# Kernel tuning notes

Hardware: AMD Instinct MI355X
Metric: run time of the kernel (lower is better)

Reference implementation:

```python
import jax, jax.numpy as jnp
import numpy as np

N, E, R, B, IN, H, OUT, P = 20000, 320000, 8, 8, 128, 256, 128, 100000
LN_EPS = 1e-5


def _xavier(key, shape):
    fan_in, fan_out = shape[-2], shape[-1]
    lim = float(np.sqrt(6.0 / (fan_in + fan_out)))
    return jax.random.uniform(key, shape, jnp.float32, -lim, lim)


def setup_inputs() -> dict:
    key = jax.random.key(0)
    ks = iter(jax.random.split(key, 64))
    inp = {}
    inp['x'] = jax.random.normal(next(ks), (N, IN), jnp.float32)
    inp['edge_index'] = jax.random.randint(next(ks), (2, E), 0, N, jnp.int32)
    inp['edge_type'] = jax.random.randint(next(ks), (E,), 0, R, jnp.int32)
    inp['gene_pairs'] = jax.random.randint(next(ks), (2, P), 0, N, jnp.int32)
    dims = [(IN, H), (H, H), (H, H), (H, OUT)]  # per-layer (in_ch, out_ch)
    for i, (ic, oc) in enumerate(dims):
        inp[f'basis{i}'] = _xavier(next(ks), (B, ic, oc))
        inp[f'att{i}'] = _xavier(next(ks), (R, B))
        inp[f'root{i}'] = _xavier(next(ks), (ic, oc))
        inp[f'relatt{i}'] = jnp.ones((R,), jnp.float32)
        inp[f'g{i}'] = jnp.ones((oc,), jnp.float32)
        inp[f'b{i}'] = jnp.zeros((oc,), jnp.float32)
    inp['res0'] = _xavier(next(ks), (IN, H))   # in_ch != out_ch at layer 0
    inp['res3'] = _xavier(next(ks), (H, OUT))  # and at layer 3
    # decoder: 3*OUT -> H -> H//2 -> H//4 -> 1
    ddims = [(3 * OUT, H), (H, H // 2), (H // 2, H // 4), (H // 4, 1)]
    for i, (ic, oc) in enumerate(ddims):
        inp[f'dW{i}'] = _xavier(next(ks), (ic, oc))
        inp[f'db{i}'] = jnp.zeros((oc,), jnp.float32)
        if i < 3:
            inp[f'dg{i}'] = jnp.ones((oc,), jnp.float32)
            inp[f'dbb{i}'] = jnp.zeros((oc,), jnp.float32)
    return inp


def _ln(h, g, b):
    m = h.mean(-1, keepdims=True)
    v = ((h - m) ** 2).mean(-1, keepdims=True)
    return (h - m) * jax.lax.rsqrt(v + LN_EPS) * g + b


def _conv(x, src, dst, et, basis, att, root_w, rel_att):
    # W_r = sum_b att[r,b] * B_b ; message = a_{r(e)} * x_src @ W_{r(e)}
    # Since the message is linear, aggregate x_src per (dst, relation) first
    # (segment_sum), then apply the R small GEMMs once - same math, no [E,in,out].
    n, d = x.shape
    weight = jnp.einsum('rb,bio->rio', att, basis)          # [R,in,out]
    a = jax.nn.softmax(rel_att)                              # [R]
    seg = dst.astype(jnp.int32) * R + et.astype(jnp.int32)   # [(node,rel)] segment ids
    agg = jax.ops.segment_sum(x[src], seg, num_segments=n * R).reshape(n, R, d)
    out = jnp.einsum('nri,rio->no', agg, weight * a[:, None, None])
    return out + x @ root_w


def reference(x, edge_index, edge_type, gene_pairs,
              basis0, att0, root0, relatt0, g0, b0, res0,
              basis1, att1, root1, relatt1, g1, b1,
              basis2, att2, root2, relatt2, g2, b2,
              basis3, att3, root3, relatt3, g3, b3, res3,
              dW0, db0, dg0, dbb0, dW1, db1, dg1, dbb1,
              dW2, db2, dg2, dbb2, dW3, db3):
    src, dst = edge_index[0], edge_index[1]
    layers = [
        (basis0, att0, root0, relatt0, g0, b0, res0),
        (basis1, att1, root1, relatt1, g1, b1, None),
        (basis2, att2, root2, relatt2, g2, b2, None),
        (basis3, att3, root3, relatt3, g3, b3, res3),
    ]
    h = x
    for i, (bs, at, rt, ra, g, b, res) in enumerate(layers):
        h_in = h
        h = _conv(h, src, dst, edge_type, bs, at, rt, ra)
        h = _ln(h, g, b)
        h = h + (h_in @ res if res is not None else h_in)
        if i < len(layers) - 1:
            h = jax.nn.gelu(h, approximate=False)
    z = h  # [N, OUT]
    zi, zj = z[gene_pairs[0]], z[gene_pairs[1]]
    pe = jnp.concatenate([zi + zj, zi * zj, jnp.abs(zi - zj)], axis=-1)
    d = jax.nn.gelu(_ln(pe @ dW0 + db0, dg0, dbb0), approximate=False)
    d = jax.nn.gelu(_ln(d @ dW1 + db1, dg1, dbb1), approximate=False)
    d = jax.nn.gelu(_ln(d @ dW2 + db2, dg2, dbb2), approximate=False)
    logits = (d @ dW3 + db3).squeeze(-1)  # [P]
    return logits, z
```

## Files before the change

kernel.cpp:

```cpp
#include <hip/hip_runtime.h>
#include <hip/hip_bf16.h>
#include <math.h>
#include <cstddef>
#include <stdint.h>

#define NN 20000
#define EE 320000
#define RR 8
#define PP 100000
#define NR (NN * RR)

typedef __hip_bfloat16 bf16;
typedef __attribute__((ext_vector_type(8))) short short8;
typedef __attribute__((ext_vector_type(4))) short short4v;
typedef __attribute__((ext_vector_type(4))) float floatx4;

__device__ __forceinline__ float b2f(bf16 v) { return __bfloat162float(v); }
__device__ __forceinline__ bf16 f2b(float v) { return __float2bfloat16(v); }
__device__ __forceinline__ float bits2f(unsigned short u) {
  unsigned int i = ((unsigned int)u) << 16; float f; __builtin_memcpy(&f, &i, 4); return f;
}
__device__ __forceinline__ short f2bits(float f) {
  bf16 h = __float2bfloat16(f); short s; __builtin_memcpy(&s, &h, 2); return s;
}
__device__ __forceinline__ float gelu_f(float y) {
  return 0.5f * y * (1.f + erff(y * 0.7071067811865476f));
}
__device__ __forceinline__ void async_copy16(void* lds, const void* g) {
  __builtin_amdgcn_global_load_lds((const __attribute__((address_space(1))) void*)g,
                                   (__attribute__((address_space(3))) void*)lds, 16, 0, 0);
}
__device__ __forceinline__ const short8* frag_at(const bf16* base, int row, int q) {
  return (const short8*)(base + row * 64 + (((q) ^ (row & 7)) << 3));
}
__device__ __forceinline__ const short8* frag256(const bf16* base, int row, int col64, int q) {
  return (const short8*)(base + row * 256 + col64 + (((q) ^ (row & 7)) << 3));
}
__device__ __forceinline__ int idx128(int row, int qg) {
  return row * 128 + ((qg >> 3) << 6) + (((qg & 7) ^ (row & 7)) << 3);
}

__global__ void hist_k(const int* __restrict__ dst, const int* __restrict__ et,
                       int* __restrict__ counts) {
  int e = blockIdx.x * 256 + threadIdx.x;
  if (e >= EE) return;
  atomicAdd(&counts[dst[e] * RR + et[e]], 1);
}

__global__ void scan1_k(const int* __restrict__ counts, int* __restrict__ prefix,
                        int* __restrict__ bsums) {
  __shared__ int tmp[256];
  int i = blockIdx.x * 256 + threadIdx.x;
  int v = counts[i];
  tmp[threadIdx.x] = v; __syncthreads();
  for (int off = 1; off < 256; off <<= 1) {
    int x = (threadIdx.x >= off) ? tmp[threadIdx.x - off] : 0;
    __syncthreads();
    tmp[threadIdx.x] += x;
    __syncthreads();
  }
  prefix[i] = tmp[threadIdx.x] - v;
  if (threadIdx.x == 255) bsums[blockIdx.x] = tmp[255];
}

__global__ void scan2_k(int* __restrict__ bsums, int nb) {
  __shared__ int tmp[256];
  __shared__ int carry;
  if (threadIdx.x == 0) carry = 0;
  __syncthreads();
  for (int base = 0; base < nb; base += 256) {
    int i = base + threadIdx.x;
    int v = (i < nb) ? bsums[i] : 0;
    tmp[threadIdx.x] = v; __syncthreads();
    for (int off = 1; off < 256; off <<= 1) {
      int x = (threadIdx.x >= off) ? tmp[threadIdx.x - off] : 0;
      __syncthreads();
      tmp[threadIdx.x] += x;
      __syncthreads();
    }
    int c = carry;
    if (i < nb) bsums[i] = c + tmp[threadIdx.x] - v;
    __syncthreads();
    if (threadIdx.x == 255) carry = c + tmp[255];
    __syncthreads();
  }
}

__global__ void scan3_k(int* __restrict__ prefix, const int* __restrict__ bsums) {
  int i = blockIdx.x * 256 + threadIdx.x;
  prefix[i] += bsums[blockIdx.x];
}

__global__ void scatter_k(const int* __restrict__ src, const int* __restrict__ dst,
                          const int* __restrict__ et, const int* __restrict__ segstart,
                          int* __restrict__ cursor, int* __restrict__ ssrc) {
  int e = blockIdx.x * 256 + threadIdx.x;
  if (e >= EE) return;
  int s = dst[e] * RR + et[e];
  int pos = atomicAdd(&cursor[s], 1);
  ssrc[segstart[s] + pos] = src[e];
}

__global__ void cvt_bf16_k(const float* __restrict__ in, bf16* __restrict__ out, int n) {
  int i = blockIdx.x * 256 + threadIdx.x;
  if (i < n) out[i] = f2b(in[i]);
}

__global__ void softmax4_k(const float* r0, const float* r1, const float* r2,
                           const float* r3, float* __restrict__ a) {
  if (threadIdx.x == 0) {
    const float* rs[4] = {r0, r1, r2, r3};
    for (int l = 0; l < 4; ++l) {
      float mx = -1e30f;
      for (int i = 0; i < RR; ++i) mx = fmaxf(mx, rs[l][i]);
      float e[RR]; float s = 0.f;
      for (int i = 0; i < RR; ++i) { e[i] = expf(rs[l][i] - mx); s += e[i]; }
      for (int i = 0; i < RR; ++i) a[l * RR + i] = e[i] / s;
    }
  }
}

__global__ void transpose_k(const float* __restrict__ in, bf16* __restrict__ out,
                            int rows, int cols) {
  int idx = blockIdx.x * 256 + threadIdx.x;
  if (idx >= rows * cols) return;
  int r = idx / cols, c = idx - r * cols;
  out[(size_t)c * rows + r] = f2b(in[idx]);
}

__global__ void prep_w_k(const float* __restrict__ basis, const float* __restrict__ att,
                         const float* __restrict__ root, const float* __restrict__ a,
                         bf16* __restrict__ Wt, int ic, int icsh, int oc, int ocsh) {
  int idx = blockIdx.x * 256 + threadIdx.x;
  int cols = 9 * ic;
  if (idx >= cols * oc) return;
  int o = idx & (oc - 1);
  int col = idx >> ocsh;
  int r = col >> icsh;
  int k = col & (ic - 1);
  float val;
  if (r < RR) {
    float acc = 0.f;
    for (int bb = 0; bb < RR; ++bb)
      acc += att[r * RR + bb] * basis[((size_t)bb * ic + k) * oc + o];
    val = a[r] * acc;
  } else {
    val = root[(size_t)k * oc + o];
  }
  Wt[(size_t)o * cols + col] = f2b(val);
}

__global__ __launch_bounds__(256) void aggregate_k(
    const bf16* __restrict__ h, const int* __restrict__ segstart,
    const int* __restrict__ counts, const int* __restrict__ ssrc,
    bf16* __restrict__ agg, int ic, int tpnsh) {
  int tpn = 1 << tpnsh;
  int npb = 256 >> tpnsh;
  int local = threadIdx.x >> tpnsh;
  int n = blockIdx.x * npb + local;
  if (n >= NN) return;
  int cbase = (threadIdx.x & (tpn - 1)) * 8;
  size_t rowoff = (size_t)n * (9 * ic);
  for (int r = 0; r < RR; ++r) {
    int s = n * RR + r;
    int st = segstart[s];
    int cnt = counts[s];
    float a[8] = {0.f, 0.f, 0.f, 0.f, 0.f, 0.f, 0.f, 0.f};
    for (int i = 0; i < cnt; ++i) {
      int src = ssrc[st + i];
      short8 v = *(const short8*)(h + (size_t)src * ic + cbase);
#pragma unroll
      for (int j = 0; j < 8; ++j) a[j] += bits2f((unsigned short)v[j]);
    }
    short8 o;
#pragma unroll
    for (int j = 0; j < 8; ++j) o[j] = f2bits(a[j]);
    *(short8*)(agg + rowoff + r * ic + cbase) = o;
  }
  *(short8*)(agg + rowoff + 8 * ic + cbase) =
      *(const short8*)(h + (size_t)n * ic + cbase);
}

__global__ __launch_bounds__(256) void gemm_f32_k(
    const bf16* __restrict__ A, const bf16* __restrict__ Wt,
    float* __restrict__ Cf, int M, int N, int K, int nb) {
  const int bid = blockIdx.x;
  const int xcd = bid & 7;
  const int slot = bid >> 3;
  const int gidx = slot / nb;
  const int member = slot - gidx * nb;
  const int mb = (M + 127) >> 7;
  const int m = gidx * 8 + xcd;
  if (m >= mb) return;
  const int m0 = m * 128;
  const int n0 = member * 64;

  __shared__ __align__(16) bf16 As[128 * 64];
  __shared__ __align__(16) bf16 Ws[64 * 64];
  const int tid = threadIdx.x;
  const int wave = tid >> 6, lane = tid & 63;
  const int quad = lane >> 4, l16 = lane & 15;
  const int wm = (wave >> 1) * 64, wn = (wave & 1) * 32;
  floatx4 acc[4][2];
#pragma unroll
  for (int i = 0; i < 4; ++i)
#pragma unroll
    for (int j = 0; j < 2; ++j) acc[i][j] = (floatx4){0.f, 0.f, 0.f, 0.f};

  for (int k0 = 0; k0 < K; k0 += 64) {
#pragma unroll
    for (int q = 0; q < 4; ++q) {
      int c0 = (wave * 4 + q) * 1024;
      int row = (c0 >> 7) + (lane >> 3);
      int grow = m0 + row; if (grow >= M) grow = M - 1;
      int ch = (lane & 7) ^ (row & 7);
      async_copy16((char*)As + c0, A + (size_t)grow * K + k0 + ch * 8);
    }
#pragma unroll
    for (int q = 0; q < 2; ++q) {
      int c0 = (wave * 2 + q) * 1024;
      int row = (c0 >> 7) + (lane >> 3);
      int ch = (lane & 7) ^ (row & 7);
      async_copy16((char*)Ws + c0, Wt + (size_t)(n0 + row) * K + k0 + ch * 8);
    }
    __syncthreads();
#pragma unroll
    for (int kk = 0; kk < 64; kk += 32) {
      int qb = (kk >> 3) + quad;
      short8 b0 = *frag_at(Ws, wn + l16, qb);
      short8 b1 = *frag_at(Ws, wn + 16 + l16, qb);
#pragma unroll
      for (int i = 0; i < 4; ++i) {
        short8 a = *frag_at(As, wm + i * 16 + l16, qb);
        acc[i][0] = __builtin_amdgcn_mfma_f32_16x16x32_bf16(a, b0, acc[i][0], 0, 0, 0);
        acc[i][1] = __builtin_amdgcn_mfma_f32_16x16x32_bf16(a, b1, acc[i][1], 0, 0, 0);
      }
    }
    __syncthreads();
  }
#pragma unroll
  for (int i = 0; i < 4; ++i)
#pragma unroll
    for (int j = 0; j < 2; ++j)
#pragma unroll
      for (int r = 0; r < 4; ++r) {
        int row = m0 + wm + i * 16 + quad * 4 + r;
        int col = n0 + wn + j * 16 + l16;
        if (row < M) Cf[(size_t)row * N + col] = acc[i][j][r];
      }
}

__global__ __launch_bounds__(256) void gemm_plain_k(
    const bf16* __restrict__ A, const bf16* __restrict__ Wt,
    bf16* __restrict__ Cb, int M, int N, int K) {
  __shared__ __align__(16) bf16 As[64 * 64];
  __shared__ __align__(16) bf16 Ws[64 * 64];
  const int m0 = blockIdx.y * 64;
  const int n0 = blockIdx.x * 64;
  const int tid = threadIdx.x;
  const int wave = tid >> 6, lane = tid & 63;
  const int quad = lane >> 4, l16 = lane & 15;
  const int wm = (wave >> 1) * 32, wn = (wave & 1) * 32;
  floatx4 acc00 = {0.f, 0.f, 0.f, 0.f};
  floatx4 acc01 = acc00, acc10 = acc00, acc11 = acc00;

  for (int k0 = 0; k0 < K; k0 += 64) {
#pragma unroll
    for (int q = 0; q < 2; ++q) {
      int c0 = (wave * 2 + q) * 1024;
      int row = (c0 >> 7) + (lane >> 3);
      int grow = m0 + row; if (grow >= M) grow = M - 1;
      int ch = (lane & 7) ^ (row & 7);
      async_copy16((char*)As + c0, A + (size_t)grow * K + k0 + ch * 8);
    }
#pragma unroll
    for (int q = 0; q < 2; ++q) {
      int c0 = (wave * 2 + q) * 1024;
      int row = (c0 >> 7) + (lane >> 3);
      int ch = (lane & 7) ^ (row & 7);
      async_copy16((char*)Ws + c0, Wt + (size_t)(n0 + row) * K + k0 + ch * 8);
    }
    __syncthreads();
#pragma unroll
    for (int kk = 0; kk < 64; kk += 32) {
      int qb = (kk >> 3) + quad;
      short8 a0 = *frag_at(As, wm + l16, qb);
      short8 a1 = *frag_at(As, wm + 16 + l16, qb);
      short8 b0 = *frag_at(Ws, wn + l16, qb);
      short8 b1 = *frag_at(Ws, wn + 16 + l16, qb);
      acc00 = __builtin_amdgcn_mfma_f32_16x16x32_bf16(a0, b0, acc00, 0, 0, 0);
      acc01 = __builtin_amdgcn_mfma_f32_16x16x32_bf16(a0, b1, acc01, 0, 0, 0);
      acc10 = __builtin_amdgcn_mfma_f32_16x16x32_bf16(a1, b0, acc10, 0, 0, 0);
      acc11 = __builtin_amdgcn_mfma_f32_16x16x32_bf16(a1, b1, acc11, 0, 0, 0);
    }
    __syncthreads();
  }
  floatx4 accs[2][2] = {{acc00, acc01}, {acc10, acc11}};
#pragma unroll
  for (int i = 0; i < 2; ++i)
#pragma unroll
    for (int j = 0; j < 2; ++j)
#pragma unroll
      for (int r = 0; r < 4; ++r) {
        int row = m0 + wm + i * 16 + quad * 4 + r;
        int col = n0 + wn + j * 16 + l16;
        if (row < M) Cb[(size_t)row * N + col] = f2b(accs[i][j][r]);
      }
}

__global__ __launch_bounds__(256) void ln_conv_k(
    const float* __restrict__ conv, const bf16* __restrict__ res,
    const float* __restrict__ g, const float* __restrict__ b,
    bf16* __restrict__ out, float* __restrict__ zout, int oc, int do_gelu) {
  int wave = threadIdx.x >> 6, lane = threadIdx.x & 63;
  int row = blockIdx.x * 4 + wave;
  if (row >= NN) return;
  int ne = oc >> 6;
  float v[4];
  float s = 0.f, s2 = 0.f;
  for (int i = 0; i < ne; ++i) {
    v[i] = conv[(size_t)row * oc + i * 64 + lane];
    s += v[i]; s2 += v[i] * v[i];
  }
  for (int off = 32; off; off >>= 1) { s += __shfl_xor(s, off); s2 += __shfl_xor(s2, off); }
  float m = s / oc;
  float var = s2 / oc - m * m;
  float rs = rsqrtf(var + 1e-5f);
  for (int i = 0; i < ne; ++i) {
    int c = i * 64 + lane;
    float y = (v[i] - m) * rs * g[c] + b[c];
    y += b2f(res[(size_t)row * oc + c]);
    if (zout) zout[(size_t)row * oc + c] = y;
    if (do_gelu) y = gelu_f(y);
    out[(size_t)row * oc + c] = f2b(y);
  }
}

__global__ __launch_bounds__(256) void gemm_pe_k(
    const bf16* __restrict__ z, const int* __restrict__ pairs,
    const bf16* __restrict__ WAT, const bf16* __restrict__ WBT,
    const bf16* __restrict__ WCT,
    bf16* __restrict__ P0) {
  __shared__ __align__(16) bf16 PEs[128 * 64];
  __shared__ __align__(16) bf16 Ws[64 * 64];
  const int tid = threadIdx.x;
  const int wave = tid >> 6, lane = tid & 63;
  const int quad = lane >> 4, l16 = lane & 15;
  const int wm = (wave >> 1) * 64, wn = (wave & 1) * 32;
  const int m0 = blockIdx.y * 128;
  const int n0 = blockIdx.x * 64;

  const int prow = tid >> 1;
  const int colq = (tid & 1) * 32;
  int pp = m0 + prow; if (pp >= PP) pp = PP - 1;
  const bf16* zi = z + (size_t)pairs[pp] * 128;
  const bf16* zj = z + (size_t)pairs[PP + pp] * 128;

  floatx4 acc[4][2];
#pragma unroll
  for (int i = 0; i < 4; ++i)
#pragma unroll
    for (int j = 0; j < 2; ++j) acc[i][j] = (floatx4){0.f, 0.f, 0.f, 0.f};

#pragma unroll
  for (int kwi = 0; kwi < 2; ++kwi) {
    const int kw = kwi * 64;
    short8 va[4], vb[4];
#pragma unroll
    for (int c8 = 0; c8 < 4; ++c8) {
      va[c8] = *(const short8*)(zi + kw + colq + c8 * 8);
      vb[c8] = *(const short8*)(zj + kw + colq + c8 * 8);
    }
#pragma unroll
    for (int op = 0; op < 3; ++op) {
      const bf16* W = (op == 0) ? WAT : (op == 1) ? WBT : WCT;
#pragma unroll
      for (int q = 0; q < 2; ++q) {
        int c0 = q * 4096 + wave * 1024;
        int row = (c0 >> 7) + (lane >> 3);
        int ch = (lane & 7) ^ (row & 7);
        async_copy16((char*)Ws + c0, W + (size_t)(n0 + row) * 128 + kw + ch * 8);
      }
#pragma unroll
      for (int c8 = 0; c8 < 4; ++c8) {
        short8 o;
#pragma unroll
        for (int jj = 0; jj < 8; ++jj) {
          float fa = bits2f((unsigned short)va[c8][jj]);
          float fb = bits2f((unsigned short)vb[c8][jj]);
          float v = (op == 0) ? (fa + fb) : (op == 1) ? (fa * fb) : fabsf(fa - fb);
          o[jj] = f2bits(v);
        }
        int q = (tid & 1) * 4 + c8;
        *(short8*)(PEs + prow * 64 + ((q ^ (prow & 7)) << 3)) = o;
      }
      __syncthreads();
#pragma unroll
      for (int kk = 0; kk < 64; kk += 32) {
        int qb = (kk >> 3) + quad;
        short8 b0 = *frag_at(Ws, wn + l16, qb);
        short8 b1 = *frag_at(Ws, wn + 16 + l16, qb);
#pragma unroll
        for (int i = 0; i < 4; ++i) {
          short8 a = *frag_at(PEs, wm + i * 16 + l16, qb);
          acc[i][0] = __builtin_amdgcn_mfma_f32_16x16x32_bf16(a, b0, acc[i][0], 0, 0, 0);
          acc[i][1] = __builtin_amdgcn_mfma_f32_16x16x32_bf16(a, b1, acc[i][1], 0, 0, 0);
        }
      }
      __syncthreads();
    }
  }

#pragma unroll
  for (int i = 0; i < 4; ++i)
#pragma unroll
    for (int j = 0; j < 2; ++j)
#pragma unroll
      for (int r = 0; r < 4; ++r) {
        int row = m0 + wm + i * 16 + quad * 4 + r;
        int col = n0 + wn + j * 16 + l16;
        if (row < PP) P0[(size_t)row * 256 + col] = f2b(acc[i][j][r]);
      }
}

__global__ __launch_bounds__(256) void ln_d0_k(bf16* __restrict__ D0,
                                               const float* __restrict__ db0,
                                               const float* __restrict__ g,
                                               const float* __restrict__ b) {
  int wave = threadIdx.x >> 6, lane = threadIdx.x & 63;
  int row = blockIdx.x * 4 + wave;
  if (row >= PP) return;
  bf16* p = D0 + (size_t)row * 256 + lane * 4;
  short4v xv = *(const short4v*)p;
  float v[4];
  float s = 0.f, s2 = 0.f;
#pragma unroll
  for (int k = 0; k < 4; ++k) {
    v[k] = bits2f((unsigned short)xv[k]) + db0[lane * 4 + k];
    s += v[k]; s2 += v[k] * v[k];
  }
  for (int off = 32; off; off >>= 1) { s += __shfl_xor(s, off); s2 += __shfl_xor(s2, off); }
  float m = s / 256.f;
  float var = s2 / 256.f - m * m;
  float rs = rsqrtf(var + 1e-5f);
  short4v ov;
#pragma unroll
  for (int k = 0; k < 4; ++k) {
    int c = lane * 4 + k;
    float y = (v[k] - m) * rs * g[c] + b[c];
    ov[k] = f2bits(gelu_f(y));
  }
  *(short4v*)p = ov;
}

__global__ __launch_bounds__(256) void lngemm1_k(
    const bf16* __restrict__ D0, const bf16* __restrict__ W1t,
    const float* __restrict__ bias, bf16* __restrict__ P1, int M) {
  __shared__ __align__(16) bf16 As[64 * 256];
  __shared__ __align__(16) bf16 Ws[128 * 64];
  const int tid = threadIdx.x;
  const int wave = tid >> 6, lane = tid & 63;
  const int quad = lane >> 4, l16 = lane & 15;
  const int wr = (wave >> 1) * 32;
  const int wc = (wave & 1) * 64;
  const int m0 = blockIdx.x * 64;

  {
    const int srow = tid >> 2;
    const int q4 = tid & 3;
    int grow = m0 + srow; if (grow >= M) grow = M - 1;
    const bf16* src = D0 + (size_t)grow * 256 + q4 * 64;
#pragma unroll
    for (int c8 = 0; c8 < 8; ++c8) {
      short8 o = *(const short8*)(src + c8 * 8);
      *(short8*)(As + srow * 256 + q4 * 64 + ((c8 ^ (srow & 7)) << 3)) = o;
    }
  }

  floatx4 acc[2][4];
#pragma unroll
  for (int i = 0; i < 2; ++i)
#pragma unroll
    for (int j = 0; j < 4; ++j) acc[i][j] = (floatx4){0.f, 0.f, 0.f, 0.f};

  for (int kc = 0; kc < 4; ++kc) {
#pragma unroll
    for (int q = 0; q < 4; ++q) {
      int c0 = q * 4096 + wave * 1024;
      int row = (c0 >> 7) + (lane >> 3);
      int ch = (lane & 7) ^ (row & 7);
      async_copy16((char*)Ws + c0, W1t + (size_t)row * 256 + kc * 64 + ch * 8);
    }
    __syncthreads();
#pragma unroll
    for (int kk = 0; kk < 64; kk += 32) {
      int qb = (kk >> 3) + quad;
      short8 a0 = *frag256(As, wr + l16, kc * 64, qb);
      short8 a1 = *frag256(As, wr + 16 + l16, kc * 64, qb);
#pragma unroll
      for (int j = 0; j < 4; ++j) {
        short8 bb = *frag_at(Ws, wc + j * 16 + l16, qb);
        acc[0][j] = __builtin_amdgcn_mfma_f32_16x16x32_bf16(a0, bb, acc[0][j], 0, 0, 0);
        acc[1][j] = __builtin_amdgcn_mfma_f32_16x16x32_bf16(a1, bb, acc[1][j], 0, 0, 0);
      }
    }
    __syncthreads();
  }

#pragma unroll
  for (int i = 0; i < 2; ++i)
#pragma unroll
    for (int r = 0; r < 4; ++r) {
      int row = wr + i * 16 + quad * 4 + r;
      int grow = m0 + row;
      if (grow >= M) continue;
#pragma unroll
      for (int j = 0; j < 4; ++j) {
        int col = wc + j * 16 + l16;
        P1[(size_t)grow * 128 + col] = f2b(acc[i][j][r] + bias[col]);
      }
    }
}

__global__ __launch_bounds__(256) void lngemm2_k(
    const bf16* __restrict__ P1, const bf16* __restrict__ W2t,
    const float* __restrict__ g, const float* __restrict__ b,
    const float* __restrict__ bias, bf16* __restrict__ P2, int M) {
  __shared__ __align__(16) bf16 As[64 * 128];
  __shared__ __align__(16) bf16 Ws[64 * 64];
  const int tid = threadIdx.x;
  const int wave = tid >> 6, lane = tid & 63;
  const int quad = lane >> 4, l16 = lane & 15;
  const int m0 = blockIdx.x * 64;

  {
    const int srow = tid >> 2;
    const int q4 = tid & 3;
    int grow = m0 + srow; if (grow >= M) grow = M - 1;
    const bf16* src = P1 + (size_t)grow * 128 + q4 * 32;
    float v[32];
    float s = 0.f, s2 = 0.f;
#pragma unroll
    for (int c8 = 0; c8 < 4; ++c8) {
      short8 x = *(const short8*)(src + c8 * 8);
#pragma unroll
      for (int jj = 0; jj < 8; ++jj) {
        float f = bits2f((unsigned short)x[jj]);
        v[c8 * 8 + jj] = f; s += f; s2 += f * f;
      }
    }
    s += __shfl_xor(s, 1); s2 += __shfl_xor(s2, 1);
    s += __shfl_xor(s, 2); s2 += __shfl_xor(s2, 2);
    float mean = s / 128.f;
    float var = s2 / 128.f - mean * mean;
    float rs = rsqrtf(var + 1e-5f);
#pragma unroll
    for (int c8 = 0; c8 < 4; ++c8) {
      short8 o;
#pragma unroll
      for (int jj = 0; jj < 8; ++jj) {
        int col = q4 * 32 + c8 * 8 + jj;
        float y = (v[c8 * 8 + jj] - mean) * rs * g[col] + b[col];
        o[jj] = f2bits(gelu_f(y));
      }
      *(short8*)(As + idx128(srow, q4 * 4 + c8)) = o;
    }
  }

  floatx4 acc[4];
#pragma unroll
  for (int j = 0; j < 4; ++j) acc[j] = (floatx4){0.f, 0.f, 0.f, 0.f};

  for (int kc = 0; kc < 2; ++kc) {
#pragma unroll
    for (int q = 0; q < 2; ++q) {
      int c0 = q * 4096 + wave * 1024;
      int row = (c0 >> 7) + (lane >> 3);
      int ch = (lane & 7) ^ (row & 7);
      async_copy16((char*)Ws + c0, W2t + (size_t)row * 128 + kc * 64 + ch * 8);
    }
    __syncthreads();
#pragma unroll
    for (int kk = 0; kk < 64; kk += 32) {
      int qb = (kk >> 3) + quad;
      short8 a = *(const short8*)(As + idx128(wave * 16 + l16, kc * 8 + qb));
#pragma unroll
      for (int j = 0; j < 4; ++j) {
        short8 bb = *frag_at(Ws, j * 16 + l16, qb);
        acc[j] = __builtin_amdgcn_mfma_f32_16x16x32_bf16(a, bb, acc[j], 0, 0, 0);
      }
    }
    __syncthreads();
  }

#pragma unroll
  for (int r = 0; r < 4; ++r) {
    int row = wave * 16 + quad * 4 + r;
    int grow = m0 + row;
    if (grow >= M) continue;
#pragma unroll
    for (int j = 0; j < 4; ++j) {
      int col = j * 16 + l16;
      P2[(size_t)grow * 64 + col] = f2b(acc[j][r] + bias[col]);
    }
  }
}

__global__ __launch_bounds__(256) void logits_k(const bf16* __restrict__ P2,
                                                const float* __restrict__ g,
                                                const float* __restrict__ b,
                                                const float* __restrict__ w3,
                                                const float* __restrict__ b3,
                                                float* __restrict__ out) {
  int wave = threadIdx.x >> 6, lane = threadIdx.x & 63;
  int p = blockIdx.x * 4 + wave;
  if (p >= PP) return;
  float v = b2f(P2[(size_t)p * 64 + lane]);
  float s = v, s2 = v * v;
  for (int off = 32; off; off >>= 1) { s += __shfl_xor(s, off); s2 += __shfl_xor(s2, off); }
  float m = s / 64.f;
  float var = s2 / 64.f - m * m;
  float rs = rsqrtf(var + 1e-5f);
  float y = gelu_f((v - m) * rs * g[lane] + b[lane]);
  float t = y * w3[lane];
  for (int off = 32; off; off >>= 1) t += __shfl_xor(t, off);
  if (lane == 0) out[p] = t + b3[0];
}

extern "C" void kernel_launch(void* const* d_in, const int* in_sizes, int n_in,
                              void* d_out, int out_size, void* d_ws, size_t ws_size,
                              hipStream_t stream) {
  auto cdiv = [](int a, int b) { return (a + b - 1) / b; };

  const float* x = (const float*)d_in[0];
  const int* ei = (const int*)d_in[1];
  const int* et = (const int*)d_in[2];
  const int* gp = (const int*)d_in[3];
  const float *basis[4], *att[4], *root[4], *relatt[4], *gln[4], *bln[4];
  for (int l = 0; l < 4; ++l) {
    basis[l]  = (const float*)d_in[4 + 6 * l];
    att[l]    = (const float*)d_in[5 + 6 * l];
    root[l]   = (const float*)d_in[6 + 6 * l];
    relatt[l] = (const float*)d_in[7 + 6 * l];
    gln[l]    = (const float*)d_in[8 + 6 * l];
    bln[l]    = (const float*)d_in[9 + 6 * l];
  }
  const float* res0 = (const float*)d_in[28];
  const float* res3 = (const float*)d_in[29];
  const float* dW0 = (const float*)d_in[30]; const float* db0 = (const float*)d_in[31];
  const float* dg0 = (const float*)d_in[32]; const float* dbb0 = (const float*)d_in[33];
  const float* dW1 = (const float*)d_in[34]; const float* db1 = (const float*)d_in[35];
  const float* dg1 = (const float*)d_in[36]; const float* dbb1 = (const float*)d_in[37];
  const float* dW2 = (const float*)d_in[38]; const float* db2 = (const float*)d_in[39];
  const float* dg2 = (const float*)d_in[40]; const float* dbb2 = (const float*)d_in[41];
  const float* dW3 = (const float*)d_in[42]; const float* db3 = (const float*)d_in[43];

  char* base = (char*)d_ws;
  size_t off = 0;
  auto alloc = [&](size_t bytes) -> char* {
    char* p = base + off;
    off += (bytes + 255) & ~(size_t)255;
    return p;
  };
  bf16* X16 = (bf16*)alloc((size_t)NN * 128 * 2);
  bf16* HA  = (bf16*)alloc((size_t)NN * 256 * 2);
  bf16* HB  = (bf16*)alloc((size_t)NN * 256 * 2);
  bf16* RESB = (bf16*)alloc((size_t)NN * 256 * 2);
  float* CONV = (float*)alloc((size_t)NN * 256 * 4);
  bf16* WT    = (bf16*)alloc((size_t)589824 * 2);
  bf16* RES0T = (bf16*)alloc((size_t)32768 * 2);
  bf16* RES3T = (bf16*)alloc((size_t)32768 * 2);
  bf16* WAT   = (bf16*)alloc((size_t)32768 * 2);
  bf16* WBT   = (bf16*)alloc((size_t)32768 * 2);
  bf16* WCT   = (bf16*)alloc((size_t)32768 * 2);
  bf16* DW1T  = (bf16*)alloc((size_t)32768 * 2);
  bf16* DW2T  = (bf16*)alloc((size_t)8192 * 2);
  float* ASOFT = (float*)alloc(32 * 4);
  int* COUNTS = (int*)alloc((size_t)NR * 4);
  int* SEG    = (int*)alloc((size_t)NR * 4);
  int* CUR    = (int*)alloc((size_t)NR * 4);
  int* BS     = (int*)alloc(1024 * 4);
  int* SSRC   = (int*)alloc((size_t)EE * 4);
  char* BIG = alloc(93000000);
  bf16* AGG = (bf16*)BIG;
  bf16* D0  = (bf16*)BIG;
  bf16* P1  = (bf16*)alloc((size_t)PP * 128 * 2);
  bf16* P2  = (bf16*)alloc((size_t)PP * 64 * 2);
  (void)ws_size; (void)in_sizes; (void)n_in; (void)out_size;

  float* out_logits = (float*)d_out;
  float* out_z = (float*)d_out + PP;

  hipMemsetAsync(COUNTS, 0, (size_t)NR * 4, stream);
  hipMemsetAsync(CUR, 0, (size_t)NR * 4, stream);
  hist_k<<<cdiv(EE, 256), 256, 0, stream>>>(ei + EE, et, COUNTS);
  scan1_k<<<NR / 256, 256, 0, stream>>>(COUNTS, SEG, BS);
  scan2_k<<<1, 256, 0, stream>>>(BS, NR / 256);
  scan3_k<<<NR / 256, 256, 0, stream>>>(SEG, BS);
  scatter_k<<<cdiv(EE, 256), 256, 0, stream>>>(ei, ei + EE, et, SEG, CUR, SSRC);

  cvt_bf16_k<<<cdiv(NN * 128, 256), 256, 0, stream>>>(x, X16, NN * 128);
  softmax4_k<<<1, 64, 0, stream>>>(relatt[0], relatt[1], relatt[2], relatt[3], ASOFT);
  transpose_k<<<cdiv(128 * 256, 256), 256, 0, stream>>>(res0, RES0T, 128, 256);
  transpose_k<<<cdiv(256 * 128, 256), 256, 0, stream>>>(res3, RES3T, 256, 128);
  transpose_k<<<cdiv(128 * 256, 256), 256, 0, stream>>>(dW0, WAT, 128, 256);
  transpose_k<<<cdiv(128 * 256, 256), 256, 0, stream>>>(dW0 + 128 * 256, WBT, 128, 256);
  transpose_k<<<cdiv(128 * 256, 256), 256, 0, stream>>>(dW0 + 256 * 256, WCT, 128, 256);
  transpose_k<<<cdiv(256 * 128, 256), 256, 0, stream>>>(dW1, DW1T, 256, 128);
  transpose_k<<<cdiv(128 * 64, 256), 256, 0, stream>>>(dW2, DW2T, 128, 64);

  const int mb = cdiv(NN, 128);
  const int swzP4 = 8 * cdiv(mb, 8) * 4;
  const int swzP2 = 8 * cdiv(mb, 8) * 2;

  prep_w_k<<<cdiv(9 * 128 * 256, 256), 256, 0, stream>>>(basis[0], att[0], root[0], ASOFT + 0, WT, 128, 7, 256, 8);
  aggregate_k<<<cdiv(NN, 16), 256, 0, stream>>>(X16, SEG, COUNTS, SSRC, AGG, 128, 4);
  gemm_plain_k<<<dim3(4, cdiv(NN, 64)), 256, 0, stream>>>(X16, RES0T, RESB, NN, 256, 128);
  gemm_f32_k<<<swzP4, 256, 0, stream>>>(AGG, WT, CONV, NN, 256, 1152, 4);
  ln_conv_k<<<cdiv(NN, 4), 256, 0, stream>>>(CONV, RESB, gln[0], bln[0], HA, nullptr, 256, 1);

  prep_w_k<<<cdiv(9 * 256 * 256, 256), 256, 0, stream>>>(basis[1], att[1], root[1], ASOFT + 8, WT, 256, 8, 256, 8);
  aggregate_k<<<cdiv(NN, 8), 256, 0, stream>>>(HA, SEG, COUNTS, SSRC, AGG, 256, 5);
  gemm_f32_k<<<swzP4, 256, 0, stream>>>(AGG, WT, CONV, NN, 256, 2304, 4);
  ln_conv_k<<<cdiv(NN, 4), 256, 0, stream>>>(CONV, HA, gln[1], bln[1], HB, nullptr, 256, 1);

  prep_w_k<<<cdiv(9 * 256 * 256, 256), 256, 0, stream>>>(basis[2], att[2], root[2], ASOFT + 16, WT, 256, 8, 256, 8);
  aggregate_k<<<cdiv(NN, 8), 256, 0, stream>>>(HB, SEG, COUNTS, SSRC, AGG, 256, 5);
  gemm_f32_k<<<swzP4, 256, 0, stream>>>(AGG, WT, CONV, NN, 256, 2304, 4);
  ln_conv_k<<<cdiv(NN, 4), 256, 0, stream>>>(CONV, HB, gln[2], bln[2], HA, nullptr, 256, 1);

  prep_w_k<<<cdiv(9 * 256 * 128, 256), 256, 0, stream>>>(basis[3], att[3], root[3], ASOFT + 24, WT, 256, 8, 128, 7);
  aggregate_k<<<cdiv(NN, 8), 256, 0, stream>>>(HA, SEG, COUNTS, SSRC, AGG, 256, 5);
  gemm_plain_k<<<dim3(2, cdiv(NN, 64)), 256, 0, stream>>>(HA, RES3T, RESB, NN, 128, 256);
  gemm_f32_k<<<swzP2, 256, 0, stream>>>(AGG, WT, CONV, NN, 128, 2304, 2);
  ln_conv_k<<<cdiv(NN, 4), 256, 0, stream>>>(CONV, RESB, gln[3], bln[3], HB, out_z, 128, 0);

  gemm_pe_k<<<dim3(4, cdiv(PP, 128)), 256, 0, stream>>>(HB, gp, WAT, WBT, WCT, D0);
  ln_d0_k<<<cdiv(PP, 4), 256, 0, stream>>>(D0, db0, dg0, dbb0);
  lngemm1_k<<<cdiv(PP, 64), 256, 0, stream>>>(D0, DW1T, db1, P1, PP);
  lngemm2_k<<<cdiv(PP, 64), 256, 0, stream>>>(P1, DW2T, dg1, dbb1, db2, P2, PP);
  logits_k<<<cdiv(PP, 4), 256, 0, stream>>>(P2, dg2, dbb2, dW3, db3, out_logits);
}
```

Baseline: 792.4 us.

## Precompute z@WA per node and remap pair-GEMM grid for XCD locality

```diff
diff --git a/kernel.cpp b/kernel.cpp
--- a/kernel.cpp
+++ b/kernel.cpp
@@ -338,17 +338,25 @@
 
 __global__ __launch_bounds__(256) void gemm_pe_k(
     const bf16* __restrict__ z, const int* __restrict__ pairs,
-    const bf16* __restrict__ WAT, const bf16* __restrict__ WBT,
-    const bf16* __restrict__ WCT,
+    const bf16* __restrict__ WBT, const bf16* __restrict__ WCT,
     bf16* __restrict__ P0) {
+  const int bid = blockIdx.x;
+  const int xcd = bid & 7;
+  const int slot = bid >> 3;
+  const int gidx = slot >> 2;
+  const int member = slot & 3;
+  const int mb = (PP + 127) >> 7;
+  const int m = gidx * 8 + xcd;
+  if (m >= mb) return;
+  const int m0 = m * 128;
+  const int n0 = member * 64;
+
   __shared__ __align__(16) bf16 PEs[128 * 64];
   __shared__ __align__(16) bf16 Ws[64 * 64];
   const int tid = threadIdx.x;
   const int wave = tid >> 6, lane = tid & 63;
   const int quad = lane >> 4, l16 = lane & 15;
   const int wm = (wave >> 1) * 64, wn = (wave & 1) * 32;
-  const int m0 = blockIdx.y * 128;
-  const int n0 = blockIdx.x * 64;
 
   const int prow = tid >> 1;
   const int colq = (tid & 1) * 32;
@@ -372,8 +380,8 @@
       vb[c8] = *(const short8*)(zj + kw + colq + c8 * 8);
     }
 #pragma unroll
-    for (int op = 0; op < 3; ++op) {
-      const bf16* W = (op == 0) ? WAT : (op == 1) ? WBT : WCT;
+    for (int op = 0; op < 2; ++op) {
+      const bf16* W = (op == 0) ? WBT : WCT;
 #pragma unroll
       for (int q = 0; q < 2; ++q) {
         int c0 = q * 4096 + wave * 1024;
@@ -388,7 +396,7 @@
         for (int jj = 0; jj < 8; ++jj) {
           float fa = bits2f((unsigned short)va[c8][jj]);
           float fb = bits2f((unsigned short)vb[c8][jj]);
-          float v = (op == 0) ? (fa + fb) : (op == 1) ? (fa * fb) : fabsf(fa - fb);
+          float v = (op == 0) ? (fa * fb) : fabsf(fa - fb);
           o[jj] = f2bits(v);
         }
         int q = (tid & 1) * 4 + c8;
@@ -424,19 +432,25 @@
 }
 
 __global__ __launch_bounds__(256) void ln_d0_k(bf16* __restrict__ D0,
+                                               const int* __restrict__ pairs,
+                                               const bf16* __restrict__ ZA,
                                                const float* __restrict__ db0,
                                                const float* __restrict__ g,
                                                const float* __restrict__ b) {
   int wave = threadIdx.x >> 6, lane = threadIdx.x & 63;
   int row = blockIdx.x * 4 + wave;
   if (row >= PP) return;
+  int gi = pairs[row], gj = pairs[PP + row];
   bf16* p = D0 + (size_t)row * 256 + lane * 4;
   short4v xv = *(const short4v*)p;
+  short4v av = *(const short4v*)(ZA + (size_t)gi * 256 + lane * 4);
+  short4v bv = *(const short4v*)(ZA + (size_t)gj * 256 + lane * 4);
   float v[4];
   float s = 0.f, s2 = 0.f;
 #pragma unroll
   for (int k = 0; k < 4; ++k) {
-    v[k] = bits2f((unsigned short)xv[k]) + db0[lane * 4 + k];
+    v[k] = bits2f((unsigned short)xv[k]) + bits2f((unsigned short)av[k]) +
+           bits2f((unsigned short)bv[k]) + db0[lane * 4 + k];
     s += v[k]; s2 += v[k] * v[k];
   }
   for (int off = 32; off; off >>= 1) { s += __shfl_xor(s, off); s2 += __shfl_xor(s2, off); }
@@ -666,6 +680,7 @@
   bf16* HA  = (bf16*)alloc((size_t)NN * 256 * 2);
   bf16* HB  = (bf16*)alloc((size_t)NN * 256 * 2);
   bf16* RESB = (bf16*)alloc((size_t)NN * 256 * 2);
+  bf16* ZA   = (bf16*)alloc((size_t)NN * 256 * 2);
   float* CONV = (float*)alloc((size_t)NN * 256 * 4);
   bf16* WT    = (bf16*)alloc((size_t)589824 * 2);
   bf16* RES0T = (bf16*)alloc((size_t)32768 * 2);
@@ -735,8 +750,11 @@
   gemm_f32_k<<<swzP2, 256, 0, stream>>>(AGG, WT, CONV, NN, 128, 2304, 2);
   ln_conv_k<<<cdiv(NN, 4), 256, 0, stream>>>(CONV, RESB, gln[3], bln[3], HB, out_z, 128, 0);
 
-  gemm_pe_k<<<dim3(4, cdiv(PP, 128)), 256, 0, stream>>>(HB, gp, WAT, WBT, WCT, D0);
-  ln_d0_k<<<cdiv(PP, 4), 256, 0, stream>>>(D0, db0, dg0, dbb0);
+  gemm_plain_k<<<dim3(4, cdiv(NN, 64)), 256, 0, stream>>>(HB, WAT, ZA, NN, 256, 128);
+  const int pb = cdiv(PP, 128);
+  const int swzPE = 8 * cdiv(pb, 8) * 4;
+  gemm_pe_k<<<swzPE, 256, 0, stream>>>(HB, gp, WBT, WCT, D0);
+  ln_d0_k<<<cdiv(PP, 4), 256, 0, stream>>>(D0, gp, ZA, db0, dg0, dbb0);
   lngemm1_k<<<cdiv(PP, 64), 256, 0, stream>>>(D0, DW1T, db1, P1, PP);
   lngemm2_k<<<cdiv(PP, 64), 256, 0, stream>>>(P1, DW2T, dg1, dbb1, db2, P2, PP);
   logits_k<<<cdiv(PP, 4), 256, 0, stream>>>(P2, dg2, dbb2, dW3, db3, out_logits);
```

Result: no change. 789.1 us (-0.4%).
